# Optimization experiments

Measured on AMD Instinct MI355X. Metric: run time of the kernel, lower is better.

Reference implementation:

```python
import jax, jax.numpy as jnp
import numpy as np
from jax import lax

B, L_IN, T, POOL = 800, 600, 45, 13  # batch, input length, pooled timesteps, pool width
HID = 160
BN_EPS = 1e-5


def _lstm_single_step(seq, w_ih, b_ih, b_hh):
    """One LSTM step from zero state, applied independently to every timestep.
    seq: [T, B, 320]; w_ih: [4H, 320]. h0=c0=0, so W_hh only contributes via b_hh.
    PyTorch gate order: i, f, g, o. c1 = sigmoid(i)*tanh(g); h1 = sigmoid(o)*tanh(c1)."""
    gates = jnp.einsum('tbc,gc->tbg', seq, w_ih) + b_ih + b_hh  # [T, B, 4H]
    i, f, g, o = jnp.split(gates, 4, axis=-1)
    c = jax.nn.sigmoid(i) * jnp.tanh(g)  # forget gate multiplies c0=0
    return jax.nn.sigmoid(o) * jnp.tanh(c)  # [T, B, H]


def setup_inputs() -> dict:
    key = jax.random.key(0)
    ks = jax.random.split(key, 16)
    s = 0.05
    return {
        'x': jax.random.normal(ks[0], (B, 4, L_IN), jnp.float32),
        'geneexpr': jax.random.normal(ks[1], (B, 19795), jnp.float32),
        'conv_w': jax.random.normal(ks[2], (320, 4, 26), jnp.float32) * s,
        'conv_b': jax.random.normal(ks[3], (320,), jnp.float32) * s,
        'w_ih_f': jax.random.normal(ks[4], (4 * HID, 320), jnp.float32) * s,
        'b_ih_f': jax.random.normal(ks[5], (4 * HID,), jnp.float32) * s,
        'b_hh_f': jax.random.normal(ks[6], (4 * HID,), jnp.float32) * s,
        'w_ih_b': jax.random.normal(ks[7], (4 * HID, 320), jnp.float32) * s,
        'b_ih_b': jax.random.normal(ks[8], (4 * HID,), jnp.float32) * s,
        'b_hh_b': jax.random.normal(ks[9], (4 * HID,), jnp.float32) * s,
        'gene_w': jax.random.normal(ks[10], (320, 19795), jnp.float32) * s,
        'gene_b': jax.random.normal(ks[11], (320,), jnp.float32) * s,
        'bn_gamma': jnp.ones((320,), jnp.float32),
        'bn_beta': jnp.zeros((320,), jnp.float32),
        'lin_w': jax.random.normal(ks[12], (925, T * 320), jnp.float32) * s,
        'lin_b': jax.random.normal(ks[13], (925,), jnp.float32) * s,
        'out_w': jax.random.normal(ks[14], (1, 925), jnp.float32) * s,
        'out_b': jax.random.normal(ks[15], (1,), jnp.float32) * s,
    }


def reference(x, geneexpr, conv_w, conv_b, w_ih_f, b_ih_f, b_hh_f,
              w_ih_b, b_ih_b, b_hh_b, gene_w, gene_b, bn_gamma, bn_beta,
              lin_w, lin_b, out_w, out_b):
    # Conv1d(4->320, k=26) + ReLU, left pad 14, MaxPool1d(13) -> 45 steps
    out = lax.conv_general_dilated(x, conv_w, (1,), 'VALID',
                                   dimension_numbers=('NCH', 'OIH', 'NCH'))
    out = jax.nn.relu(out + conv_b[None, :, None])          # [B, 320, 575]
    out = jnp.pad(out, ((0, 0), (0, 0), (14, 0)))           # [B, 320, 589]
    out = out[:, :, :T * POOL].reshape(B, 320, T, POOL).max(-1)  # [B, 320, 45]
    seq = out.transpose(2, 0, 1)                             # [T, B, 320]

    # Per-timestep single-step bidirectional LSTM from zero state (hidden reset each step)
    h_f = _lstm_single_step(seq, w_ih_f, b_ih_f, b_hh_f)     # [T, B, 160]
    h_b = _lstm_single_step(seq, w_ih_b, b_ih_b, b_hh_b)     # [T, B, 160]
    h = jnp.concatenate([h_f, h_b], axis=-1)                 # [T, B, 320]

    # gene expression projection + BatchNorm1d (batch stats, training forward) + ReLU
    gene = geneexpr @ gene_w.T + gene_b                      # [B, 320]
    mean = gene.mean(0)
    var = gene.var(0)  # biased, as torch BN normalization
    gene = jax.nn.relu((gene - mean) / jnp.sqrt(var + BN_EPS) * bn_gamma + bn_beta)

    # attention: dot product of each step's hidden with gene vector
    attn = jnp.einsum('tbd,bd->tb', h, gene)                 # [T, B]
    weighted = attn[:, :, None] * h                          # [T, B, 320]
    flat = weighted.transpose(1, 0, 2).reshape(B, T * 320)   # [B, 14400]

    hid = jax.nn.relu(flat @ lin_w.T + lin_b)                # [B, 925]
    return hid @ out_w.T + out_b                             # [B, 1]
```

## Files before the change

kernel.cpp:

```cpp
#include <hip/hip_runtime.h>
#include <hip/hip_bf16.h>
#include <math.h>

#define BB   800
#define CIN  4
#define XLEN 600
#define COUT 320
#define KW   26
#define TT   45
#define HID  160
#define LSTM_N 1280
#define LSTM_K 320
#define LSTM_M 36000
#define GENE_K 19795
#define GENE_N 320
#define LIN_K 14400
#define LIN_N 925
#define GENE_SPLITS 24
#define LIN_SPLITS 8

#define OFF_H      ((size_t)0)
#define OFF_BP     ((size_t)5760000)
#define OFF_BIAS   ((size_t)5964800)
#define OFF_WD     ((size_t)5966080)
#define OFF_GENE   ((size_t)15820960)
#define OFF_STATS  ((size_t)16076960)
#define OFF_ATTN   ((size_t)16077600)
#define OFF_HID    ((size_t)16113600)
#define OFF_SCR    ((size_t)16853600)
#define OFF_SEQS   ((size_t)22997600)

typedef __attribute__((ext_vector_type(8))) _Float16 half8v;
typedef __attribute__((ext_vector_type(8))) unsigned short ushort8v;
typedef __attribute__((ext_vector_type(4))) float f32x4;
typedef __attribute__((ext_vector_type(4))) unsigned uint4v;

__device__ __forceinline__ float sigf(float x) { return 1.0f / (1.0f + __expf(-x)); }
__device__ __forceinline__ float tanhfast(float x) { return 2.0f / (1.0f + __expf(-2.0f * x)) - 1.0f; }

__device__ __forceinline__ unsigned short f16rne(float f) {
    _Float16 h = (_Float16)f;
    return __builtin_bit_cast(unsigned short, h);
}
__device__ __forceinline__ float f16tof(unsigned short u) {
    return (float)__builtin_bit_cast(_Float16, u);
}

__device__ __forceinline__ ushort8v lds_window8(const unsigned short* chbase, int off) {
    const unsigned short* ap = chbase + (off & ~7);
    uint4 A = *reinterpret_cast<const uint4*>(ap);
    uint4 Bv = *reinterpret_cast<const uint4*>(ap + 8);
    int s = off & 7;
    bool hi4 = s >= 4;
    unsigned e0 = hi4 ? A.z : A.x;
    unsigned e1 = hi4 ? A.w : A.y;
    unsigned e2 = hi4 ? Bv.x : A.z;
    unsigned e3 = hi4 ? Bv.y : A.w;
    unsigned e4 = hi4 ? Bv.z : Bv.x;
    unsigned e5 = hi4 ? Bv.w : Bv.y;
    int s2 = s & 3;
    int bsh = s2 * 16;
    unsigned o0 = (unsigned)((((unsigned long long)e1 << 32) | e0) >> bsh);
    unsigned o1 = (unsigned)((((unsigned long long)e2 << 32) | e1) >> bsh);
    unsigned o2 = (unsigned)((((unsigned long long)e3 << 32) | e2) >> bsh);
    unsigned o3 = (unsigned)((((unsigned long long)e4 << 32) | e3) >> bsh);
    if (s2 == 3) {
        o0 |= e2 << 16;
        o1 |= e3 << 16;
        o2 |= e4 << 16;
        o3 |= e5 << 16;
    }
    uint4v o = {o0, o1, o2, o3};
    return *reinterpret_cast<ushort8v*>(&o);
}

__global__ void prep_lstm_kernel(const float* __restrict__ wf, const float* __restrict__ bif,
                                 const float* __restrict__ bhf,
                                 const float* __restrict__ wb, const float* __restrict__ bib,
                                 const float* __restrict__ bhb,
                                 unsigned short* __restrict__ Bp, float* __restrict__ biasv) {
    int idx = blockIdx.x * 256 + threadIdx.x;
    if (idx < LSTM_N * LSTM_K) {
        int n = idx / LSTM_K, k = idx % LSTM_K;
        int dir = n / 640, r = n % 640;
        int jg = r >> 6, rr = r & 63, gate = rr >> 4, jl = rr & 15;
        int srow = gate * HID + jg * 16 + jl;
        const float* w = dir ? wb : wf;
        Bp[idx] = f16rne(w[(size_t)srow * LSTM_K + k]);
    }
    if (idx < LSTM_N) {
        int n = idx;
        int dir = n / 640, r = n % 640;
        int jg = r >> 6, rr = r & 63, gate = rr >> 4, jl = rr & 15;
        int srow = gate * HID + jg * 16 + jl;
        biasv[n] = dir ? (bib[srow] + bhb[srow]) : (bif[srow] + bhf[srow]);
    }
}

__global__ void prep_convw_kernel(const float* __restrict__ cw, unsigned short* __restrict__ wd) {
    int idx = blockIdx.x * 256 + threadIdx.x;
    if (idx < COUT * 128) {
        int c = idx >> 7, k = idx & 127;
        int ch = k >> 5, kk = k & 31;
        wd[idx] = (kk < KW) ? f16rne(cw[(size_t)c * 104 + ch * KW + kk]) : (unsigned short)0;
    }
}

#define CST 130

__global__ __launch_bounds__(256, 3) void conv_mfma_kernel(const float* __restrict__ x,
                                                           const unsigned short* __restrict__ wd,
                                                           const float* __restrict__ cb,
                                                           unsigned short* __restrict__ seqs) {
    __shared__ __align__(16) unsigned char smem[34560];
    float* Csh = (float*)smem;
    unsigned short* xraw = (unsigned short*)(smem + 33280);

    int bx = blockIdx.x;
    int b = bx / 5, wt = bx % 5;
    int col0 = blockIdx.y * 128;
    int p0 = 117 * wt - 14;
    int tid = threadIdx.x;

    const int w = tid >> 6, lane = tid & 63;
    const int wr = w >> 1, wc = w & 1;
    const int l15 = lane & 15, lq = lane >> 4;

    ushort8v bA[4], bB[4];
#pragma unroll
    for (int n = 0; n < 4; ++n) {
        int cg = col0 + wc * 64 + n * 16 + l15;
        cg = min(cg, COUT - 1);
        bA[n] = *reinterpret_cast<const ushort8v*>(wd + (size_t)cg * 128 + 0 * 32 + lq * 8);
    }

    {
        const float* xb = x + (size_t)b * (CIN * XLEN);
        if (wt >= 1 && wt <= 3) {
            for (int j = tid; j < 4 * 160; j += 256) {
                int ch = j / 160, i = j - ch * 160;
                float v = (i < 154) ? xb[ch * XLEN + p0 + i] : 0.0f;
                xraw[ch * 160 + i] = f16rne(v);
            }
        } else {
            for (int j = tid; j < 4 * 160; j += 256) {
                int ch = j / 160, i = j - ch * 160;
                int p = p0 + i;
                float v = (i < 154 && p >= 0 && p < XLEN) ? xb[ch * XLEN + p] : 0.0f;
                xraw[ch * 160 + i] = f16rne(v);
            }
        }
    }
    __syncthreads();

    f32x4 acc[4][4];
#pragma unroll
    for (int m = 0; m < 4; ++m)
#pragma unroll
        for (int n = 0; n < 4; ++n) acc[m][n] = (f32x4){0.f, 0.f, 0.f, 0.f};

#pragma unroll
    for (int ks = 0; ks < 4; ++ks) {
        const ushort8v* bcur = (ks & 1) ? bB : bA;
        ushort8v* bnext = (ks & 1) ? bA : bB;
        if (ks < 3) {
#pragma unroll
            for (int n = 0; n < 4; ++n) {
                int cg = col0 + wc * 64 + n * 16 + l15;
                cg = min(cg, COUT - 1);
                bnext[n] = *reinterpret_cast<const ushort8v*>(
                    wd + (size_t)cg * 128 + (ks + 1) * 32 + lq * 8);
            }
        }
        const unsigned short* chb = xraw + ks * 160;
#pragma unroll
        for (int m = 0; m < 4; ++m) {
            ushort8v afu = lds_window8(chb, wr * 64 + m * 16 + l15 + lq * 8);
#pragma unroll
            for (int n = 0; n < 4; ++n)
                acc[m][n] = __builtin_amdgcn_mfma_f32_16x16x32_f16(
                    *reinterpret_cast<const half8v*>(&afu),
                    *reinterpret_cast<const half8v*>(&bcur[n]), acc[m][n], 0, 0, 0);
        }
    }

    float pu4 = -1.0e30f;

    if (wr == 0) {
#pragma unroll
        for (int m = 0; m < 4; ++m)
#pragma unroll
            for (int n = 0; n < 4; ++n)
#pragma unroll
                for (int rg = 0; rg < 4; ++rg) {
                    int row = m * 16 + lq * 4 + rg;
                    int col = wc * 64 + n * 16 + l15;
                    Csh[row * CST + col] = acc[m][n][rg];
                }
    }
    __syncthreads();

#pragma unroll
    for (int i = 0; i < 2; ++i) {
        int j = i * 256 + tid;
        int u = j >> 7, c = j & 127;
        int cg = col0 + c;
        float mx = -1.0e30f;
        if (wt == 0) {
#pragma unroll
            for (int jj = 0; jj < 13; ++jj) {
                int r = 13 * u + jj;
                if (r >= 14) mx = fmaxf(mx, Csh[r * CST + c]);
            }
        } else {
#pragma unroll
            for (int jj = 0; jj < 13; ++jj) {
                int r = 13 * u + jj;
                mx = fmaxf(mx, Csh[r * CST + c]);
            }
        }
        if (cg < COUT) {
            float v = fmaxf(mx + cb[cg], 0.0f);
            seqs[((size_t)(wt * 9 + u) * BB + b) * 320 + cg] = f16rne(v);
        }
    }
    if (tid < 128) {
        int c = tid;
#pragma unroll
        for (int jj = 0; jj < 12; ++jj) pu4 = fmaxf(pu4, Csh[(52 + jj) * CST + c]);
    }
    __syncthreads();

    if (wr == 1) {
#pragma unroll
        for (int m = 0; m < 4; ++m)
#pragma unroll
            for (int n = 0; n < 4; ++n)
#pragma unroll
                for (int rg = 0; rg < 4; ++rg) {
                    int row = m * 16 + lq * 4 + rg;
                    int col = wc * 64 + n * 16 + l15;
                    Csh[row * CST + col] = acc[m][n][rg];
                }
    }
    __syncthreads();

#pragma unroll
    for (int i = 0; i < 2; ++i) {
        int j = i * 256 + tid;
        int u = 5 + (j >> 7), c = j & 127;
        int cg = col0 + c;
        float mx = -1.0e30f;
#pragma unroll
        for (int jj = 0; jj < 13; ++jj) {
            int r = 13 * u + jj;
            mx = fmaxf(mx, Csh[(r - 64) * CST + c]);
        }
        if (cg < COUT) {
            float v = fmaxf(mx + cb[cg], 0.0f);
            seqs[((size_t)(wt * 9 + u) * BB + b) * 320 + cg] = f16rne(v);
        }
    }
    if (tid < 128) {
        int c = tid;
        int cg = col0 + c;
        pu4 = fmaxf(pu4, Csh[0 * CST + c]);
        if (cg < COUT) {
            float v = fmaxf(pu4 + cb[cg], 0.0f);
            seqs[((size_t)(wt * 9 + 4) * BB + b) * 320 + cg] = f16rne(v);
        }
    }
}

template <int VAR, bool BF32>
__global__ __launch_bounds__(256) void gemm2(const unsigned short* __restrict__ Apre,
                                             const float* __restrict__ Af32, int lda,
                                             const unsigned short* __restrict__ Bn,
                                             const float* __restrict__ Bf32, int ldb,
                                             const float* __restrict__ attnp,
                                             int M, int N, int Kreal,
                                             int totChunks, int cps,
                                             float* __restrict__ outp,
                                             const float* __restrict__ biasv,
                                             unsigned short* __restrict__ hout) {
    __shared__ unsigned short Al[128][72];
    __shared__ unsigned short Bl[128][72];
    const int tid = threadIdx.x;

    int bm, bn, sp;
    if (VAR == 0) {
        int xcd = blockIdx.x;
        bn = blockIdx.y % 10;
        bm = xcd + 8 * (blockIdx.y / 10);
        sp = 0;
        if (bm >= 282) return;
    } else if (VAR == 1) {
        int xcd = blockIdx.x;
        sp = xcd + 8 * (blockIdx.y / 21);
        int r = blockIdx.y % 21;
        bm = r / 3; bn = r % 3;
    } else {
        sp = blockIdx.x;
        bn = blockIdx.y / 7; bm = blockIdx.y % 7;
    }
    const int row0 = bm * 128, col0 = bn * 128;
    const int c_beg = sp * cps;
    const int c_end = min(totChunks, c_beg + cps);

    const int w = tid >> 6, lane = tid & 63;
    const int wr = w >> 1, wc = w & 1;
    const int l15 = lane & 15, lq = lane >> 4;

    f32x4 acc[4][4];
#pragma unroll
    for (int m = 0; m < 4; ++m)
#pragma unroll
        for (int n = 0; n < 4; ++n) acc[m][n] = (f32x4){0.f, 0.f, 0.f, 0.f};

    ushort8v aP[4];
    float4 aF[8];
    float aW[4];
    ushort8v bP[4];
    float4 bF[8];

    auto loadA = [&](int c) {
        int k0 = c * 64;
        if (VAR == 0) {
#pragma unroll
            for (int i = 0; i < 4; ++i) {
                int j = tid + i * 256;
                int r = j >> 3, kg = j & 7;
                int gr = row0 + r;
                ushort8v z = {0, 0, 0, 0, 0, 0, 0, 0};
                if (gr < M) z = *reinterpret_cast<const ushort8v*>(
                    Apre + (size_t)gr * 320 + k0 + kg * 8);
                aP[i] = z;
            }
        } else if (VAR == 1) {
            bool fast = (k0 + 64 <= Kreal);
#pragma unroll
            for (int i = 0; i < 4; ++i) {
                int j = tid + i * 256;
                int r = j >> 3, kg = j & 7;
                int gr = row0 + r;
                float4 v0 = make_float4(0.f, 0.f, 0.f, 0.f);
                float4 v1 = make_float4(0.f, 0.f, 0.f, 0.f);
                if (gr < M) {
                    int kb = k0 + kg * 8;
                    const float* p = Af32 + (size_t)gr * lda + kb;
                    if (fast) {
                        v0 = *reinterpret_cast<const float4*>(p);
                        v1 = *reinterpret_cast<const float4*>(p + 4);
                    } else {
                        if (kb + 0 < Kreal) v0.x = p[0];
                        if (kb + 1 < Kreal) v0.y = p[1];
                        if (kb + 2 < Kreal) v0.z = p[2];
                        if (kb + 3 < Kreal) v0.w = p[3];
                        if (kb + 4 < Kreal) v1.x = p[4];
                        if (kb + 5 < Kreal) v1.y = p[5];
                        if (kb + 6 < Kreal) v1.z = p[6];
                        if (kb + 7 < Kreal) v1.w = p[7];
                    }
                }
                aF[2 * i] = v0; aF[2 * i + 1] = v1;
            }
        } else {
            int t = k0 / 320, d0 = k0 - t * 320;
#pragma unroll
            for (int i = 0; i < 4; ++i) {
                int j = tid + i * 256;
                int r = j >> 3, kg = j & 7;
                int gr = row0 + r;
                ushort8v z = {0, 0, 0, 0, 0, 0, 0, 0};
                float aw = 0.0f;
                if (gr < M) {
                    z = *reinterpret_cast<const ushort8v*>(
                        Apre + ((size_t)t * BB + gr) * 320 + d0 + kg * 8);
                    aw = attnp[t * BB + gr];
                }
                aP[i] = z; aW[i] = aw;
            }
        }
    };
    auto loadB = [&](int c) {
        int k0 = c * 64;
        if (BF32) {
            bool fast = (k0 + 64 <= Kreal);
#pragma unroll
            for (int i = 0; i < 4; ++i) {
                int j = tid + i * 256;
                int r = j >> 3, kg = j & 7;
                int gc = col0 + r;
                float4 v0 = make_float4(0.f, 0.f, 0.f, 0.f);
                float4 v1 = make_float4(0.f, 0.f, 0.f, 0.f);
                if (gc < N) {
                    int kb = k0 + kg * 8;
                    const float* p = Bf32 + (size_t)gc * ldb + kb;
                    if (fast) {
                        v0 = *reinterpret_cast<const float4*>(p);
                        v1 = *reinterpret_cast<const float4*>(p + 4);
                    } else {
                        if (kb + 0 < Kreal) v0.x = p[0];
                        if (kb + 1 < Kreal) v0.y = p[1];
                        if (kb + 2 < Kreal) v0.z = p[2];
                        if (kb + 3 < Kreal) v0.w = p[3];
                        if (kb + 4 < Kreal) v1.x = p[4];
                        if (kb + 5 < Kreal) v1.y = p[5];
                        if (kb + 6 < Kreal) v1.z = p[6];
                        if (kb + 7 < Kreal) v1.w = p[7];
                    }
                }
                bF[2 * i] = v0; bF[2 * i + 1] = v1;
            }
        } else {
#pragma unroll
            for (int i = 0; i < 4; ++i) {
                int j = tid + i * 256;
                int r = j >> 3, sg = j & 7;
                int gc = col0 + r;
                ushort8v z = {0, 0, 0, 0, 0, 0, 0, 0};
                if (gc < N) z = *reinterpret_cast<const ushort8v*>(Bn + (size_t)gc * ldb + k0 + sg * 8);
                bP[i] = z;
            }
        }
    };
    auto writeAB = [&]() {
        if (VAR == 0) {
#pragma unroll
            for (int i = 0; i < 4; ++i) {
                int j = tid + i * 256;
                int r = j >> 3, kg = j & 7;
                *reinterpret_cast<ushort8v*>(&Al[r][kg * 8]) = aP[i];
            }
        } else {
#pragma unroll
            for (int i = 0; i < 4; ++i) {
                int j = tid + i * 256;
                int r = j >> 3, kg = j & 7;
                ushort8v hv;
                if (VAR == 1) {
                    hv[0] = f16rne(aF[2 * i].x); hv[1] = f16rne(aF[2 * i].y);
                    hv[2] = f16rne(aF[2 * i].z); hv[3] = f16rne(aF[2 * i].w);
                    hv[4] = f16rne(aF[2 * i + 1].x); hv[5] = f16rne(aF[2 * i + 1].y);
                    hv[6] = f16rne(aF[2 * i + 1].z); hv[7] = f16rne(aF[2 * i + 1].w);
                } else {
#pragma unroll
                    for (int e = 0; e < 8; ++e) hv[e] = f16rne(f16tof(aP[i][e]) * aW[i]);
                }
                *reinterpret_cast<ushort8v*>(&Al[r][kg * 8]) = hv;
            }
        }
        if (BF32) {
#pragma unroll
            for (int i = 0; i < 4; ++i) {
                int j = tid + i * 256;
                int r = j >> 3, kg = j & 7;
                ushort8v hv;
                hv[0] = f16rne(bF[2 * i].x); hv[1] = f16rne(bF[2 * i].y);
                hv[2] = f16rne(bF[2 * i].z); hv[3] = f16rne(bF[2 * i].w);
                hv[4] = f16rne(bF[2 * i + 1].x); hv[5] = f16rne(bF[2 * i + 1].y);
                hv[6] = f16rne(bF[2 * i + 1].z); hv[7] = f16rne(bF[2 * i + 1].w);
                *reinterpret_cast<ushort8v*>(&Bl[r][kg * 8]) = hv;
            }
        } else {
#pragma unroll
            for (int i = 0; i < 4; ++i) {
                int j = tid + i * 256;
                int r = j >> 3, sg = j & 7;
                *reinterpret_cast<ushort8v*>(&Bl[r][sg * 8]) = bP[i];
            }
        }
    };

    loadA(c_beg); loadB(c_beg);

    for (int c = c_beg; c < c_end; ++c) {
        __syncthreads();
        writeAB();
        __syncthreads();
        if (c + 1 < c_end) { loadA(c + 1); loadB(c + 1); }

#pragma unroll
        for (int ks = 0; ks < 2; ++ks) {
            half8v bf[4];
#pragma unroll
            for (int n = 0; n < 4; ++n)
                bf[n] = *reinterpret_cast<const half8v*>(&Bl[wc * 64 + n * 16 + l15][ks * 32 + lq * 8]);
            half8v af[4];
#pragma unroll
            for (int m = 0; m < 4; ++m)
                af[m] = *reinterpret_cast<const half8v*>(&Al[wr * 64 + m * 16 + l15][ks * 32 + lq * 8]);
#pragma unroll
            for (int m = 0; m < 4; ++m)
#pragma unroll
                for (int n = 0; n < 4; ++n)
                    acc[m][n] = __builtin_amdgcn_mfma_f32_16x16x32_f16(af[m], bf[n], acc[m][n], 0, 0, 0);
        }
    }

    if (VAR != 0) {
#pragma unroll
        for (int m = 0; m < 4; ++m)
#pragma unroll
            for (int n = 0; n < 4; ++n)
#pragma unroll
                for (int rg = 0; rg < 4; ++rg) {
                    int row_g = row0 + wr * 64 + m * 16 + lq * 4 + rg;
                    int col_g = col0 + wc * 64 + n * 16 + l15;
                    if (row_g < M && col_g < N)
                        outp[((size_t)sp * M + row_g) * N + col_g] = acc[m][n][rg];
                }
    } else {
        int c0 = col0 + wc * 64;
        int dir = c0 / 640;
        int jgl = (c0 % 640) >> 6;
        int hcol = dir * HID + jgl * 16 + l15;
        float bi = biasv[c0 + l15];
        float bg = biasv[c0 + 32 + l15];
        float bo = biasv[c0 + 48 + l15];
#pragma unroll
        for (int m = 0; m < 4; ++m)
#pragma unroll
            for (int rg = 0; rg < 4; ++rg) {
                int row_g = row0 + wr * 64 + m * 16 + lq * 4 + rg;
                if (row_g >= M) continue;
                float gi = acc[m][0][rg] + bi;
                float gg = acc[m][2][rg] + bg;
                float go = acc[m][3][rg] + bo;
                float cc = sigf(gi) * tanhfast(gg);
                hout[(size_t)row_g * 320 + hcol] = f16rne(sigf(go) * tanhfast(cc));
            }
    }
}

__global__ void gene_reduce_kernel(const float* __restrict__ part, const float* __restrict__ gene_b,
                                   float* __restrict__ out) {
    int idx = blockIdx.x * 256 + threadIdx.x;
    if (idx >= BB * GENE_N) return;
    int n = idx % GENE_N;
    float sum = gene_b[n];
#pragma unroll
    for (int ss = 0; ss < GENE_SPLITS; ++ss) sum += part[(size_t)ss * (BB * GENE_N) + idx];
    out[idx] = sum;
}

__global__ void bn_stats_kernel(const float* __restrict__ g, float* __restrict__ stats) {
    int n = blockIdx.x;
    int tid = threadIdx.x;
    float s = 0.0f, s2 = 0.0f;
    for (int m = tid; m < BB; m += 256) {
        float v = g[(size_t)m * GENE_N + n];
        s += v; s2 += v * v;
    }
    __shared__ float red0[256], red1[256];
    red0[tid] = s; red1[tid] = s2;
    __syncthreads();
    for (int off = 128; off; off >>= 1) {
        if (tid < off) { red0[tid] += red0[tid + off]; red1[tid] += red1[tid + off]; }
        __syncthreads();
    }
    if (tid == 0) {
        float mean = red0[0] / (float)BB;
        float var = red1[0] / (float)BB - mean * mean;
        stats[n] = mean;
        stats[GENE_N + n] = rsqrtf(var + 1e-5f);
    }
}

__global__ void attn_kernel(const unsigned short* __restrict__ h, const float* __restrict__ graw,
                            const float* __restrict__ stats,
                            const float* __restrict__ gamma, const float* __restrict__ beta,
                            float* __restrict__ attn) {
    int r = blockIdx.x * 4 + (threadIdx.x >> 6);
    int b = r % BB;
    int lane = threadIdx.x & 63;
    const unsigned short* hr = h + (size_t)r * 320;
    const float* gr = graw + (size_t)b * 320;
    float s = 0.0f;
    for (int d = lane; d < 320; d += 64) {
        float gv = (gr[d] - stats[d]) * stats[GENE_N + d] * gamma[d] + beta[d];
        gv = fmaxf(gv, 0.0f);
        s += f16tof(hr[d]) * gv;
    }
    for (int off = 32; off; off >>= 1) s += __shfl_down(s, off);
    if (lane == 0) attn[r] = s;
}

__global__ void lin_reduce_kernel(const float* __restrict__ part, const float* __restrict__ lin_b,
                                  float* __restrict__ hid) {
    int idx = blockIdx.x * 256 + threadIdx.x;
    if (idx >= BB * LIN_N) return;
    int n = idx % LIN_N;
    float sum = lin_b[n];
#pragma unroll
    for (int ss = 0; ss < LIN_SPLITS; ++ss) sum += part[(size_t)ss * (BB * LIN_N) + idx];
    hid[idx] = fmaxf(sum, 0.0f);
}

__global__ void out_kernel(const float* __restrict__ hid, const float* __restrict__ ow,
                           const float* __restrict__ ob, float* __restrict__ out) {
    int b = blockIdx.x;
    int lane = threadIdx.x;
    float s = 0.0f;
    for (int n = lane; n < LIN_N; n += 64) s += hid[(size_t)b * LIN_N + n] * ow[n];
    for (int off = 32; off; off >>= 1) s += __shfl_down(s, off);
    if (lane == 0) out[b] = s + ob[0];
}

extern "C" void kernel_launch(void* const* d_in, const int* in_sizes, int n_in,
                              void* d_out, int out_size, void* d_ws, size_t ws_size,
                              hipStream_t stream) {
    const float* x        = (const float*)d_in[0];
    const float* geneexpr = (const float*)d_in[1];
    const float* conv_w   = (const float*)d_in[2];
    const float* conv_b   = (const float*)d_in[3];
    const float* w_ih_f   = (const float*)d_in[4];
    const float* b_ih_f   = (const float*)d_in[5];
    const float* b_hh_f   = (const float*)d_in[6];
    const float* w_ih_b   = (const float*)d_in[7];
    const float* b_ih_b   = (const float*)d_in[8];
    const float* b_hh_b   = (const float*)d_in[9];
    const float* gene_w   = (const float*)d_in[10];
    const float* gene_b   = (const float*)d_in[11];
    const float* bn_gamma = (const float*)d_in[12];
    const float* bn_beta  = (const float*)d_in[13];
    const float* lin_w    = (const float*)d_in[14];
    const float* lin_b    = (const float*)d_in[15];
    const float* out_w    = (const float*)d_in[16];
    const float* out_b    = (const float*)d_in[17];

    float* ws  = (float*)d_ws;
    float* out = (float*)d_out;

    unsigned short* h     = (unsigned short*)(ws + OFF_H);
    unsigned short* Bp    = (unsigned short*)(ws + OFF_BP);
    float* biasv          = ws + OFF_BIAS;
    unsigned short* wd    = (unsigned short*)(ws + OFF_WD);
    float* gene           = ws + OFF_GENE;
    float* stats          = ws + OFF_STATS;
    float* attn           = ws + OFF_ATTN;
    float* hid            = ws + OFF_HID;
    float* gpart          = ws + OFF_SCR;
    float* lpart          = ws + OFF_SCR;
    unsigned short* seqs  = (unsigned short*)(ws + OFF_SEQS);

    prep_lstm_kernel<<<1600, 256, 0, stream>>>(w_ih_f, b_ih_f, b_hh_f,
                                               w_ih_b, b_ih_b, b_hh_b, Bp, biasv);
    prep_convw_kernel<<<160, 256, 0, stream>>>(conv_w, wd);
    conv_mfma_kernel<<<dim3(BB * 5, 3, 1), 256, 0, stream>>>(x, wd, conv_b, seqs);
    gemm2<0, false><<<dim3(8, 360), 256, 0, stream>>>(
        seqs, nullptr, 0, Bp, nullptr, LSTM_K, nullptr,
        LSTM_M, LSTM_N, LSTM_K, 5, 5, nullptr, biasv, h);
    gemm2<1, true><<<dim3(8, 63), 256, 0, stream>>>(
        nullptr, geneexpr, GENE_K, nullptr, gene_w, GENE_K, nullptr,
        BB, GENE_N, GENE_K, 310, 13, gpart, nullptr, nullptr);
    gene_reduce_kernel<<<1000, 256, 0, stream>>>(gpart, gene_b, gene);
    bn_stats_kernel<<<GENE_N, 256, 0, stream>>>(gene, stats);
    attn_kernel<<<9000, 256, 0, stream>>>(h, gene, stats, bn_gamma, bn_beta, attn);
    gemm2<2, true><<<dim3(8, 56), 256, 0, stream>>>(
        h, nullptr, 0, nullptr, lin_w, LIN_K, attn,
        BB, LIN_N, LIN_K, 225, 29, lpart, nullptr, nullptr);
    lin_reduce_kernel<<<2891, 256, 0, stream>>>(lpart, lin_b, hid);
    out_kernel<<<BB, 64, 0, stream>>>(hid, out_w, out_b, out);
}
```

Before: 303.4 us.

## Loop conv over all channel tiles per block and max-pool in registers

The conv kernel now runs all three 128-channel tiles inside one block instead of launching a grid dimension per tile. The input window is staged in LDS once and reused across tiles. Max-pooling happens directly on accumulator registers using cross-lane shuffles, which removes the large LDS staging buffer and most barriers. Only the pool window that straddles the two row halves is combined through a small shared array. The block count drops threefold and each block does more serial work, which lowers parallelism but frees LDS for higher occupancy.

```diff
diff --git a/kernel.cpp b/kernel.cpp
--- a/kernel.cpp
+++ b/kernel.cpp
@@ -106,33 +106,22 @@
     }
 }
 
-#define CST 130
-
 __global__ __launch_bounds__(256, 3) void conv_mfma_kernel(const float* __restrict__ x,
                                                            const unsigned short* __restrict__ wd,
                                                            const float* __restrict__ cb,
                                                            unsigned short* __restrict__ seqs) {
-    __shared__ __align__(16) unsigned char smem[34560];
-    float* Csh = (float*)smem;
-    unsigned short* xraw = (unsigned short*)(smem + 33280);
+    __shared__ __align__(16) unsigned short xraw[4 * 160];
+    __shared__ float u4a[3][128];
+    __shared__ float u4b[3][128];
 
     int bx = blockIdx.x;
     int b = bx / 5, wt = bx % 5;
-    int col0 = blockIdx.y * 128;
     int p0 = 117 * wt - 14;
     int tid = threadIdx.x;
 
     const int w = tid >> 6, lane = tid & 63;
     const int wr = w >> 1, wc = w & 1;
     const int l15 = lane & 15, lq = lane >> 4;
-
-    ushort8v bA[4], bB[4];
-#pragma unroll
-    for (int n = 0; n < 4; ++n) {
-        int cg = col0 + wc * 64 + n * 16 + l15;
-        cg = min(cg, COUT - 1);
-        bA[n] = *reinterpret_cast<const ushort8v*>(wd + (size_t)cg * 128 + 0 * 32 + lq * 8);
-    }
 
     {
         const float* xb = x + (size_t)b * (CIN * XLEN);
@@ -153,120 +142,107 @@
     }
     __syncthreads();
 
-    f32x4 acc[4][4];
-#pragma unroll
-    for (int m = 0; m < 4; ++m)
-#pragma unroll
-        for (int n = 0; n < 4; ++n) acc[m][n] = (f32x4){0.f, 0.f, 0.f, 0.f};
-
-#pragma unroll
-    for (int ks = 0; ks < 4; ++ks) {
-        const ushort8v* bcur = (ks & 1) ? bB : bA;
-        ushort8v* bnext = (ks & 1) ? bA : bB;
-        if (ks < 3) {
+    const bool pad0 = (wt == 0) && (wr == 0);
+
+    for (int ct = 0; ct < 3; ++ct) {
+        int col0 = ct << 7;
+
+        ushort8v bA[4], bB[4];
+#pragma unroll
+        for (int n = 0; n < 4; ++n) {
+            int cg = col0 + wc * 64 + n * 16 + l15;
+            cg = min(cg, COUT - 1);
+            bA[n] = *reinterpret_cast<const ushort8v*>(wd + (size_t)cg * 128 + lq * 8);
+        }
+
+        f32x4 acc[4][4];
+#pragma unroll
+        for (int m = 0; m < 4; ++m)
+#pragma unroll
+            for (int n = 0; n < 4; ++n) acc[m][n] = (f32x4){0.f, 0.f, 0.f, 0.f};
+
+#pragma unroll
+        for (int ks = 0; ks < 4; ++ks) {
+            const ushort8v* bcur = (ks & 1) ? bB : bA;
+            ushort8v* bnext = (ks & 1) ? bA : bB;
+            if (ks < 3) {
+#pragma unroll
+                for (int n = 0; n < 4; ++n) {
+                    int cg = col0 + wc * 64 + n * 16 + l15;
+                    cg = min(cg, COUT - 1);
+                    bnext[n] = *reinterpret_cast<const ushort8v*>(
+                        wd + (size_t)cg * 128 + (ks + 1) * 32 + lq * 8);
+                }
+            }
+            const unsigned short* chb = xraw + ks * 160;
+#pragma unroll
+            for (int m = 0; m < 4; ++m) {
+                ushort8v afu = lds_window8(chb, wr * 64 + m * 16 + l15 + lq * 8);
+#pragma unroll
+                for (int n = 0; n < 4; ++n)
+                    acc[m][n] = __builtin_amdgcn_mfma_f32_16x16x32_f16(
+                        *reinterpret_cast<const half8v*>(&afu),
+                        *reinterpret_cast<const half8v*>(&bcur[n]), acc[m][n], 0, 0, 0);
+            }
+        }
+
+#pragma unroll
+        for (int u = 0; u < 4; ++u) {
+            int gu = wr ? (5 + u) : u;
+            int lo = 13 * gu - wr * 64;
+            int hi = lo + 13;
+            if (pad0 && lo < 14) lo = 14;
 #pragma unroll
             for (int n = 0; n < 4; ++n) {
-                int cg = col0 + wc * 64 + n * 16 + l15;
-                cg = min(cg, COUT - 1);
-                bnext[n] = *reinterpret_cast<const ushort8v*>(
-                    wd + (size_t)cg * 128 + (ks + 1) * 32 + lq * 8);
-            }
-        }
-        const unsigned short* chb = xraw + ks * 160;
-#pragma unroll
-        for (int m = 0; m < 4; ++m) {
-            ushort8v afu = lds_window8(chb, wr * 64 + m * 16 + l15 + lq * 8);
-#pragma unroll
-            for (int n = 0; n < 4; ++n)
-                acc[m][n] = __builtin_amdgcn_mfma_f32_16x16x32_f16(
-                    *reinterpret_cast<const half8v*>(&afu),
-                    *reinterpret_cast<const half8v*>(&bcur[n]), acc[m][n], 0, 0, 0);
-        }
-    }
-
-    float pu4 = -1.0e30f;
-
-    if (wr == 0) {
-#pragma unroll
-        for (int m = 0; m < 4; ++m)
-#pragma unroll
-            for (int n = 0; n < 4; ++n)
-#pragma unroll
-                for (int rg = 0; rg < 4; ++rg) {
-                    int row = m * 16 + lq * 4 + rg;
-                    int col = wc * 64 + n * 16 + l15;
-                    Csh[row * CST + col] = acc[m][n][rg];
+                float mx = -1.0e30f;
+#pragma unroll
+                for (int m = 0; m < 4; ++m)
+#pragma unroll
+                    for (int rg = 0; rg < 4; ++rg) {
+                        int lr = m * 16 + lq * 4 + rg;
+                        if (lr >= lo && lr < hi) mx = fmaxf(mx, acc[m][n][rg]);
+                    }
+                mx = fmaxf(mx, __shfl_xor(mx, 16));
+                mx = fmaxf(mx, __shfl_xor(mx, 32));
+                if (lq == 0) {
+                    int cg = col0 + wc * 64 + n * 16 + l15;
+                    if (cg < COUT) {
+                        float v = fmaxf(mx + cb[cg], 0.0f);
+                        seqs[((size_t)(wt * 9 + gu) * BB + b) * 320 + cg] = f16rne(v);
+                    }
                 }
+            }
+        }
+        if (wr == 0) {
+#pragma unroll
+            for (int n = 0; n < 4; ++n) {
+                float mx = -1.0e30f;
+#pragma unroll
+                for (int m = 0; m < 4; ++m)
+#pragma unroll
+                    for (int rg = 0; rg < 4; ++rg) {
+                        int lr = m * 16 + lq * 4 + rg;
+                        if (lr >= 52) mx = fmaxf(mx, acc[m][n][rg]);
+                    }
+                mx = fmaxf(mx, __shfl_xor(mx, 16));
+                mx = fmaxf(mx, __shfl_xor(mx, 32));
+                if (lq == 0) u4a[ct][wc * 64 + n * 16 + l15] = mx;
+            }
+        } else {
+            if (lq == 0) {
+#pragma unroll
+                for (int n = 0; n < 4; ++n)
+                    u4b[ct][wc * 64 + n * 16 + l15] = acc[0][n][0];
+            }
+        }
     }
     __syncthreads();
 
-#pragma unroll
-    for (int i = 0; i < 2; ++i) {
-        int j = i * 256 + tid;
-        int u = j >> 7, c = j & 127;
-        int cg = col0 + c;
-        float mx = -1.0e30f;
-        if (wt == 0) {
-#pragma unroll
-            for (int jj = 0; jj < 13; ++jj) {
-                int r = 13 * u + jj;
-                if (r >= 14) mx = fmaxf(mx, Csh[r * CST + c]);
-            }
-        } else {
-#pragma unroll
-            for (int jj = 0; jj < 13; ++jj) {
-                int r = 13 * u + jj;
-                mx = fmaxf(mx, Csh[r * CST + c]);
-            }
-        }
+    for (int j = tid; j < 3 * 128; j += 256) {
+        int ct = j >> 7, c = j & 127;
+        int cg = ct * 128 + c;
         if (cg < COUT) {
-            float v = fmaxf(mx + cb[cg], 0.0f);
-            seqs[((size_t)(wt * 9 + u) * BB + b) * 320 + cg] = f16rne(v);
-        }
-    }
-    if (tid < 128) {
-        int c = tid;
-#pragma unroll
-        for (int jj = 0; jj < 12; ++jj) pu4 = fmaxf(pu4, Csh[(52 + jj) * CST + c]);
-    }
-    __syncthreads();
-
-    if (wr == 1) {
-#pragma unroll
-        for (int m = 0; m < 4; ++m)
-#pragma unroll
-            for (int n = 0; n < 4; ++n)
-#pragma unroll
-                for (int rg = 0; rg < 4; ++rg) {
-                    int row = m * 16 + lq * 4 + rg;
-                    int col = wc * 64 + n * 16 + l15;
-                    Csh[row * CST + col] = acc[m][n][rg];
-                }
-    }
-    __syncthreads();
-
-#pragma unroll
-    for (int i = 0; i < 2; ++i) {
-        int j = i * 256 + tid;
-        int u = 5 + (j >> 7), c = j & 127;
-        int cg = col0 + c;
-        float mx = -1.0e30f;
-#pragma unroll
-        for (int jj = 0; jj < 13; ++jj) {
-            int r = 13 * u + jj;
-            mx = fmaxf(mx, Csh[(r - 64) * CST + c]);
-        }
-        if (cg < COUT) {
-            float v = fmaxf(mx + cb[cg], 0.0f);
-            seqs[((size_t)(wt * 9 + u) * BB + b) * 320 + cg] = f16rne(v);
-        }
-    }
-    if (tid < 128) {
-        int c = tid;
-        int cg = col0 + c;
-        pu4 = fmaxf(pu4, Csh[0 * CST + c]);
-        if (cg < COUT) {
-            float v = fmaxf(pu4 + cb[cg], 0.0f);
+            float v = fmaxf(fmaxf(u4a[ct][c], u4b[ct][c]) + cb[cg], 0.0f);
             seqs[((size_t)(wt * 9 + 4) * BB + b) * 320 + cg] = f16rne(v);
         }
     }
@@ -647,7 +623,7 @@
     prep_lstm_kernel<<<1600, 256, 0, stream>>>(w_ih_f, b_ih_f, b_hh_f,
                                                w_ih_b, b_ih_b, b_hh_b, Bp, biasv);
     prep_convw_kernel<<<160, 256, 0, stream>>>(conv_w, wd);
-    conv_mfma_kernel<<<dim3(BB * 5, 3, 1), 256, 0, stream>>>(x, wd, conv_b, seqs);
+    conv_mfma_kernel<<<dim3(BB * 5), 256, 0, stream>>>(x, wd, conv_b, seqs);
     gemm2<0, false><<<dim3(8, 360), 256, 0, stream>>>(
         seqs, nullptr, 0, Bp, nullptr, LSTM_K, nullptr,
         LSTM_M, LSTM_N, LSTM_K, 5, 5, nullptr, biasv, h);
```

New measurement: 900.4 us. 197% more time.
